# Kernel optimization log

Hardware: AMD Instinct MI355X
Metric: run time of the kernel (lower is better)

Reference implementation:

```python
import jax, jax.numpy as jnp
import numpy as np

B, L, H, E, R = 2, 512, 768, 512, 32768
H2 = H // 2


def setup_inputs() -> dict:
    key = jax.random.key(0)
    ks = jax.random.split(key, 16)
    s = 0.02
    inp = {
        "hidden_states": jax.random.normal(ks[0], (B, L, H), dtype=jnp.float32),
        "ent_start": jax.random.randint(ks[1], (B, E), 0, L, dtype=jnp.int32),
        "ent_label": jax.random.randint(ks[2], (B, E), 0, 3, dtype=jnp.int32),
        "rel_head": jax.random.randint(ks[3], (B, R), 0, E, dtype=jnp.int32),
        "rel_tail": jax.random.randint(ks[4], (B, R), 0, E, dtype=jnp.int32),
        "rel_label": jax.random.randint(ks[5], (B, R), 0, 2, dtype=jnp.int32),
        "entity_emb": jax.random.normal(ks[6], (3, H), dtype=jnp.float32) * s,
        "head_W1": jax.random.normal(ks[7], (2 * H, H), dtype=jnp.float32) * s,
        "head_b1": jnp.zeros((H,), dtype=jnp.float32),
        "head_W2": jax.random.normal(ks[8], (H, H2), dtype=jnp.float32) * s,
        "head_b2": jnp.zeros((H2,), dtype=jnp.float32),
        "tail_W1": jax.random.normal(ks[9], (2 * H, H), dtype=jnp.float32) * s,
        "tail_b1": jnp.zeros((H,), dtype=jnp.float32),
        "tail_W2": jax.random.normal(ks[10], (H, H2), dtype=jnp.float32) * s,
        "tail_b2": jnp.zeros((H2,), dtype=jnp.float32),
        "bil_W": jax.random.normal(ks[11], (2, H2, H2), dtype=jnp.float32) * s,
        "lin_W": jax.random.normal(ks[12], (2 * H2, 2), dtype=jnp.float32) * s,
        "lin_b": jnp.zeros((2,), dtype=jnp.float32),
    }
    return inp


def _mlp(x, W1, b1, W2, b2):
    # Linear -> ReLU -> (dropout=identity) -> Linear -> ReLU -> (dropout=identity)
    h = jax.nn.relu(jnp.einsum("brd,dh->brh", x, W1) + b1)
    return jax.nn.relu(jnp.einsum("brh,hk->brk", h, W2) + b2)


def reference(hidden_states, ent_start, ent_label, rel_head, rel_tail, rel_label,
              entity_emb, head_W1, head_b1, head_W2, head_b2,
              tail_W1, tail_b1, tail_W2, tail_b2, bil_W, lin_W, lin_b):
    # Gather entity start token index and label for each relation endpoint
    h_idx = jnp.take_along_axis(ent_start, rel_head, axis=1)  # [B,R]
    t_idx = jnp.take_along_axis(ent_start, rel_tail, axis=1)
    h_lab = jnp.take_along_axis(ent_label, rel_head, axis=1)
    t_lab = jnp.take_along_axis(ent_label, rel_tail, axis=1)

    # Gather hidden states at entity start positions: [B,R,H]
    h_tok = jnp.take_along_axis(hidden_states, h_idx[..., None], axis=1)
    t_tok = jnp.take_along_axis(hidden_states, t_idx[..., None], axis=1)

    head_repr = jnp.concatenate([h_tok, entity_emb[h_lab]], axis=-1)  # [B,R,2H]
    tail_repr = jnp.concatenate([t_tok, entity_emb[t_lab]], axis=-1)

    heads = _mlp(head_repr, head_W1, head_b1, head_W2, head_b2)  # [B,R,H2]
    tails = _mlp(tail_repr, tail_W1, tail_b1, tail_W2, tail_b2)

    # BiaffineAttention: bilinear(x1,x2) + linear(cat(x1,x2))
    bil = jnp.einsum("brd,ode,bre->bro", heads, bil_W, tails)  # [B,R,2]
    lin = jnp.einsum("brc,co->bro", jnp.concatenate([heads, tails], axis=-1), lin_W) + lin_b
    logits = bil + lin  # [B,R,2]

    # Per-doc mean cross-entropy, summed over docs (matches loss accumulation)
    logp = jax.nn.log_softmax(logits, axis=-1)
    ce = -jnp.take_along_axis(logp, rel_label[..., None], axis=-1)[..., 0]  # [B,R]
    loss = ce.mean(axis=-1).sum()

    return loss, logits.reshape(B * R, 2)
```

## Files before the change

### kernel.cpp

```cpp
#include <hip/hip_runtime.h>
#include <math.h>

#define BB 2
#define LL 512
#define HH 768
#define EE 512
#define RR 32768
#define H2 384
#define MM 1024

typedef __attribute__((ext_vector_type(8))) short     bf16x8;
typedef __attribute__((ext_vector_type(4))) float     f32x4;
typedef __attribute__((ext_vector_type(8))) unsigned short u16x8;

__device__ __forceinline__ unsigned short f2bf(float f) {
    unsigned int u = __float_as_uint(f);
    u = (u + 0x7FFFu + ((u >> 16) & 1u)) >> 16;
    return (unsigned short)u;
}

__global__ __launch_bounds__(256) void prep(
    const float* __restrict__ hW1, const float* __restrict__ tW1,
    const float* __restrict__ hW2, const float* __restrict__ tW2,
    const float* __restrict__ bilW,
    unsigned short* __restrict__ W1ht, unsigned short* __restrict__ W1tt,
    unsigned short* __restrict__ W2ht, unsigned short* __restrict__ W2tt,
    unsigned short* __restrict__ bW0t, unsigned short* __restrict__ bW1t,
    const float* __restrict__ hidden, const int* __restrict__ ent_start,
    const int* __restrict__ ent_label, const float* __restrict__ emb,
    const float* __restrict__ hb1, const float* __restrict__ tb1,
    unsigned short* __restrict__ Hbf, float* __restrict__ embc,
    float* __restrict__ hlin, float* __restrict__ tlin, float* __restrict__ out)
{
    __shared__ unsigned short T[32 * 40];
    __shared__ float red[4][192];
    const int bid = blockIdx.x;
    const int t = threadIdx.x;

    if (bid == 3064) {
        const float4 z = {0.f, 0.f, 0.f, 0.f};
        ((float4*)hlin)[t] = z; ((float4*)hlin)[256 + t] = z;
        ((float4*)tlin)[t] = z; ((float4*)tlin)[256 + t] = z;
        if (t == 0) out[0] = 0.f;
        return;
    }

    if (bid >= 3040) {
        const int eb = bid - 3040;
        const int tc = t & 63;
        const int kg = t >> 6;
        const int n = eb * 64 + tc;
        const float* W = (n < 768) ? hW1 : tW1;
        const int cc = (n < 768) ? n : n - 768;
        float a0 = 0.f, a1 = 0.f, a2 = 0.f;
        const int kbeg = kg * 192;
        #pragma unroll 8
        for (int k = kbeg; k < kbeg + 192; ++k) {
            const float w = W[(size_t)(768 + k) * 768 + cc];
            a0 += emb[k] * w;
            a1 += emb[768 + k] * w;
            a2 += emb[1536 + k] * w;
        }
        red[kg][0 * 64 + tc] = a0;
        red[kg][1 * 64 + tc] = a1;
        red[kg][2 * 64 + tc] = a2;
        __syncthreads();
        if (kg == 0) {
            const float b = (n < 768) ? hb1[n] : tb1[n - 768];
            #pragma unroll
            for (int l = 0; l < 3; ++l) {
                embc[l * 1536 + n] = b + red[0][l * 64 + tc] + red[1][l * 64 + tc]
                                       + red[2][l * 64 + tc] + red[3][l * 64 + tc];
            }
        }
        return;
    }

    if (bid >= 2016) {
        const int m = bid - 2016;
        if (t >= 96) return;
        const int b = m >> 9;
        const int idx = ent_start[m];
        const float4* s = (const float4*)(hidden + (size_t)(b * LL + idx) * HH);
        const float4 v0 = s[2 * t];
        const float4 v1 = s[2 * t + 1];
        u16x8 o;
        o[0] = f2bf(v0.x); o[1] = f2bf(v0.y); o[2] = f2bf(v0.z); o[3] = f2bf(v0.w);
        o[4] = f2bf(v1.x); o[5] = f2bf(v1.y); o[6] = f2bf(v1.z); o[7] = f2bf(v1.w);
        *(u16x8*)(Hbf + (size_t)m * 768 + 8 * t) = o;
        return;
    }

    const float* src; unsigned short* dst; int K, N, tile;
    if (bid < 576)       { src = hW1;            dst = W1ht; K = 768; N = 768; tile = bid; }
    else if (bid < 1152) { src = tW1;            dst = W1tt; K = 768; N = 768; tile = bid - 576; }
    else if (bid < 1440) { src = hW2;            dst = W2ht; K = 768; N = 384; tile = bid - 1152; }
    else if (bid < 1728) { src = tW2;            dst = W2tt; K = 768; N = 384; tile = bid - 1440; }
    else if (bid < 1872) { src = bilW;           dst = bW0t; K = 384; N = 384; tile = bid - 1728; }
    else                 { src = bilW + 384*384; dst = bW1t; K = 384; N = 384; tile = bid - 1872; }
    const int tn = N >> 5;
    const int n0 = (tile % tn) * 32;
    const int k0 = (tile / tn) * 32;

    const int r  = t >> 3;
    const int c4 = (t & 7) * 4;
    const float4 g = *(const float4*)(src + (size_t)(k0 + r) * N + n0 + c4);
    T[(c4 + 0) * 40 + r] = f2bf(g.x);
    T[(c4 + 1) * 40 + r] = f2bf(g.y);
    T[(c4 + 2) * 40 + r] = f2bf(g.z);
    T[(c4 + 3) * 40 + r] = f2bf(g.w);
    __syncthreads();
    const int n  = t >> 3;
    const int k4 = (t & 7) * 4;
    *(ushort4*)(dst + (size_t)(n0 + n) * K + k0 + k4) = *(ushort4*)&T[n * 40 + k4];
}

template<bool RELU, bool BIAS, bool EB, bool WF32, bool WBF16, bool O2, bool LIN>
__global__ __launch_bounds__(256) void gemm_mfma(
    const unsigned short* __restrict__ A, int lda, int aoff1,
    const unsigned short* __restrict__ Bt0, const unsigned short* __restrict__ Bt1,
    int ldb, int bt_mrow, int Nh,
    const float* __restrict__ bias0, const float* __restrict__ bias1,
    const float* __restrict__ embc, const int* __restrict__ labels,
    const float* __restrict__ linW, float* __restrict__ hlin, float* __restrict__ tlin,
    int K, float* __restrict__ Cf, unsigned short* __restrict__ Cb, int ldc)
{
    __shared__ unsigned short As[2][64 * 72];
    __shared__ unsigned short Bs[2][64 * 72];

    const int tid = threadIdx.x;
    const int n0 = blockIdx.x * 64;
    const int m0 = blockIdx.y * 64;
    const int hf = (n0 >= Nh) ? 1 : 0;
    const unsigned short* Bt = hf ? Bt1 : Bt0;
    const int nc0 = n0 - (hf ? Nh : 0);
    const int aoff = hf ? aoff1 : 0;

    const int sr = tid >> 2;
    const int sk = (tid & 3) * 16;

    const unsigned short* Ap = A + (size_t)(m0 + sr) * lda + aoff + sk;
    const unsigned short* Bp = Bt + (size_t)((m0 >> 9) * bt_mrow + nc0 + sr) * ldb + sk;

    const int lane = tid & 63;
    const int wave = tid >> 6;
    const int wm = (wave & 1) * 32;
    const int wn = (wave >> 1) * 32;
    const int l15 = lane & 15;
    const int quad = lane >> 4;

    f32x4 acc00 = {}, acc01 = {}, acc10 = {}, acc11 = {};

    u16x8 a0v = *(const u16x8*)(Ap);
    u16x8 a1v = *(const u16x8*)(Ap + 8);
    u16x8 b0v = *(const u16x8*)(Bp);
    u16x8 b1v = *(const u16x8*)(Bp + 8);
    const int swo = sr * 72 + sk;
    *(u16x8*)&As[0][swo] = a0v; *(u16x8*)&As[0][swo + 8] = a1v;
    *(u16x8*)&Bs[0][swo] = b0v; *(u16x8*)&Bs[0][swo + 8] = b1v;

    const int NT = K >> 6;
    const int aro = quad * 8;
    int cur = 0;
    for (int it = 0; it < NT; ++it) {
        if (it + 1 < NT) {
            const int ko = (it + 1) * 64;
            a0v = *(const u16x8*)(Ap + ko); a1v = *(const u16x8*)(Ap + ko + 8);
            b0v = *(const u16x8*)(Bp + ko); b1v = *(const u16x8*)(Bp + ko + 8);
        }
        asm volatile("s_waitcnt lgkmcnt(0)" ::: "memory");
        __builtin_amdgcn_s_barrier();
        __builtin_amdgcn_sched_barrier(0);
        const unsigned short* Ac = As[cur];
        const unsigned short* Bc = Bs[cur];
        const bf16x8 fa0 = *(const bf16x8*)&Ac[(wm + l15) * 72 + aro];
        const bf16x8 fa1 = *(const bf16x8*)&Ac[(wm + 16 + l15) * 72 + aro];
        const bf16x8 fb0 = *(const bf16x8*)&Bc[(wn + l15) * 72 + aro];
        const bf16x8 fb1 = *(const bf16x8*)&Bc[(wn + 16 + l15) * 72 + aro];
        const bf16x8 ga0 = *(const bf16x8*)&Ac[(wm + l15) * 72 + aro + 32];
        const bf16x8 ga1 = *(const bf16x8*)&Ac[(wm + 16 + l15) * 72 + aro + 32];
        const bf16x8 gb0 = *(const bf16x8*)&Bc[(wn + l15) * 72 + aro + 32];
        const bf16x8 gb1 = *(const bf16x8*)&Bc[(wn + 16 + l15) * 72 + aro + 32];
        acc00 = __builtin_amdgcn_mfma_f32_16x16x32_bf16(fa0, fb0, acc00, 0, 0, 0);
        acc01 = __builtin_amdgcn_mfma_f32_16x16x32_bf16(fa0, fb1, acc01, 0, 0, 0);
        acc10 = __builtin_amdgcn_mfma_f32_16x16x32_bf16(fa1, fb0, acc10, 0, 0, 0);
        acc11 = __builtin_amdgcn_mfma_f32_16x16x32_bf16(fa1, fb1, acc11, 0, 0, 0);
        acc00 = __builtin_amdgcn_mfma_f32_16x16x32_bf16(ga0, gb0, acc00, 0, 0, 0);
        acc01 = __builtin_amdgcn_mfma_f32_16x16x32_bf16(ga0, gb1, acc01, 0, 0, 0);
        acc10 = __builtin_amdgcn_mfma_f32_16x16x32_bf16(ga1, gb0, acc10, 0, 0, 0);
        acc11 = __builtin_amdgcn_mfma_f32_16x16x32_bf16(ga1, gb1, acc11, 0, 0, 0);
        if (it + 1 < NT) {
            unsigned short* Aw = &As[cur ^ 1][0];
            unsigned short* Bw = &Bs[cur ^ 1][0];
            *(u16x8*)&Aw[swo] = a0v; *(u16x8*)&Aw[swo + 8] = a1v;
            *(u16x8*)&Bw[swo] = b0v; *(u16x8*)&Bw[swo + 8] = b1v;
        }
        cur ^= 1;
    }

    float bias_v0 = 0.f, bias_v1 = 0.f;
    if (BIAS) {
        const float* bb = hf ? bias1 : bias0;
        bias_v0 = bb[nc0 + wn + l15];
        bias_v1 = bb[nc0 + wn + 16 + l15];
    }
    const int col0 = n0 + wn + l15;
    const int col1 = col0 + 16;
    int colw0 = col0, colw1 = col1;
    if (O2) {
        colw0 = 2 * (nc0 + wn + l15) + hf;
        colw1 = 2 * (nc0 + wn + 16 + l15) + hf;
    }
    float2 lw0 = {0.f, 0.f}, lw1 = {0.f, 0.f};
    float* lout = nullptr;
    if (LIN) {
        lw0 = ((const float2*)linW)[col0];
        lw1 = ((const float2*)linW)[col1];
        lout = hf ? tlin : hlin;
    }
    const f32x4 accs[2][2] = {{acc00, acc01}, {acc10, acc11}};
    #pragma unroll
    for (int mi = 0; mi < 2; ++mi) {
        #pragma unroll
        for (int r = 0; r < 4; ++r) {
            const int row = m0 + wm + mi * 16 + quad * 4 + r;
            float v0 = accs[mi][0][r];
            float v1 = accs[mi][1][r];
            if (BIAS) { v0 += bias_v0; v1 += bias_v1; }
            if (EB) {
                const int lab = labels[row];
                v0 += embc[lab * 1536 + col0];
                v1 += embc[lab * 1536 + col1];
            }
            if (RELU) { v0 = fmaxf(v0, 0.f); v1 = fmaxf(v1, 0.f); }
            if (WF32) {
                Cf[(size_t)row * ldc + colw0] = v0;
                Cf[(size_t)row * ldc + colw1] = v1;
            }
            if (WBF16) {
                Cb[(size_t)row * ldc + colw0] = f2bf(v0);
                Cb[(size_t)row * ldc + colw1] = f2bf(v1);
            }
            if (LIN) {
                float s0 = v0 * lw0.x + v1 * lw1.x;
                float s1 = v0 * lw0.y + v1 * lw1.y;
                #pragma unroll
                for (int o = 8; o >= 1; o >>= 1) {
                    s0 += __shfl_xor(s0, o, 64);
                    s1 += __shfl_xor(s1, o, 64);
                }
                if (l15 == 0) {
                    atomicAdd(&lout[2 * row],     s0);
                    atomicAdd(&lout[2 * row + 1], s1);
                }
            }
        }
    }
}

__global__ __launch_bounds__(256) void rel_gather(
    const float* __restrict__ Stab,
    const float* __restrict__ hlin, const float* __restrict__ tlin,
    const float* __restrict__ lin_b,
    const int* __restrict__ rel_head, const int* __restrict__ rel_tail,
    const int* __restrict__ rel_label,
    float* __restrict__ out)
{
    const int tid = threadIdx.x;
    const int i = blockIdx.x * 256 + tid;
    const int b = i >> 15;
    const int h = rel_head[i];
    const int t = rel_tail[i];
    const int lab = rel_label[i];
    const int mh = (b << 9) + h;
    const int mt = (b << 9) + t;

    const float2 hl = ((const float2*)hlin)[mh];
    const float2 tl = ((const float2*)tlin)[mt];
    const float2 zz = *(const float2*)(Stab + (size_t)mh * 1024 + 2 * t);
    const float z0 = zz.x + hl.x + tl.x + lin_b[0];
    const float z1 = zz.y + hl.y + tl.y + lin_b[1];
    out[1 + 2 * (size_t)i]     = z0;
    out[2 + 2 * (size_t)i]     = z1;

    const float mx = fmaxf(z0, z1);
    const float mn = fminf(z0, z1);
    const float lse = mx + log1pf(expf(mn - mx));
    float ce = lse - (lab ? z1 : z0);

    #pragma unroll
    for (int o = 32; o >= 1; o >>= 1) ce += __shfl_xor(ce, o, 64);
    __shared__ float wsum[4];
    if ((tid & 63) == 0) wsum[tid >> 6] = ce;
    __syncthreads();
    if (tid == 0) {
        const float bs = wsum[0] + wsum[1] + wsum[2] + wsum[3];
        atomicAdd(out, bs * (1.0f / (float)RR));
    }
}

extern "C" void kernel_launch(void* const* d_in, const int* in_sizes, int n_in,
                              void* d_out, int out_size, void* d_ws, size_t ws_size,
                              hipStream_t stream) {
    const float* hidden    = (const float*)d_in[0];
    const int*   ent_start = (const int*)d_in[1];
    const int*   ent_label = (const int*)d_in[2];
    const int*   rel_head  = (const int*)d_in[3];
    const int*   rel_tail  = (const int*)d_in[4];
    const int*   rel_label = (const int*)d_in[5];
    const float* emb       = (const float*)d_in[6];
    const float* head_W1   = (const float*)d_in[7];
    const float* head_b1   = (const float*)d_in[8];
    const float* head_W2   = (const float*)d_in[9];
    const float* head_b2   = (const float*)d_in[10];
    const float* tail_W1   = (const float*)d_in[11];
    const float* tail_b1   = (const float*)d_in[12];
    const float* tail_W2   = (const float*)d_in[13];
    const float* tail_b2   = (const float*)d_in[14];
    const float* bil_W     = (const float*)d_in[15];
    const float* lin_W     = (const float*)d_in[16];
    const float* lin_b     = (const float*)d_in[17];
    float* out = (float*)d_out;

    char* w = (char*)d_ws;
    auto carve = [&](size_t bytes) {
        char* p = w; w += (bytes + 255) & ~(size_t)255; return p;
    };
    unsigned short* Hbf  = (unsigned short*)carve((size_t)MM * 768 * 2);
    unsigned short* Y1bf = (unsigned short*)carve((size_t)MM * 1536 * 2);
    unsigned short* HTbf = (unsigned short*)carve((size_t)MM * 768 * 2);
    unsigned short* hWbf = (unsigned short*)carve((size_t)MM * 768 * 2);
    float*          Stab = (float*)carve((size_t)MM * 1024 * 4);
    unsigned short* W1ht = (unsigned short*)carve((size_t)768 * 768 * 2);
    unsigned short* W1tt = (unsigned short*)carve((size_t)768 * 768 * 2);
    unsigned short* W2ht = (unsigned short*)carve((size_t)384 * 768 * 2);
    unsigned short* W2tt = (unsigned short*)carve((size_t)384 * 768 * 2);
    unsigned short* bW0t = (unsigned short*)carve((size_t)384 * 384 * 2);
    unsigned short* bW1t = (unsigned short*)carve((size_t)384 * 384 * 2);
    float*          embc = (float*)carve((size_t)3 * 1536 * 4);
    float*          hlin = (float*)carve(2048 * 4);
    float*          tlin = (float*)carve(2048 * 4);

    prep<<<3065, 256, 0, stream>>>(
        head_W1, tail_W1, head_W2, tail_W2, bil_W,
        W1ht, W1tt, W2ht, W2tt, bW0t, bW1t,
        hidden, ent_start, ent_label, emb, head_b1, tail_b1, Hbf, embc,
        hlin, tlin, out);

    gemm_mfma<true, false, true, false, true, false, false>
        <<<dim3(24, 16), 256, 0, stream>>>(
        Hbf, 768, 0, W1ht, W1tt, 768, 0, 768, nullptr, nullptr, embc, ent_label,
        nullptr, nullptr, nullptr, 768, nullptr, Y1bf, 1536);

    gemm_mfma<true, true, false, false, true, false, true>
        <<<dim3(12, 16), 256, 0, stream>>>(
        Y1bf, 1536, 768, W2ht, W2tt, 768, 0, 384, head_b2, tail_b2, nullptr, nullptr,
        lin_W, hlin, tlin, 768, nullptr, HTbf, 768);

    gemm_mfma<false, false, false, false, true, false, false>
        <<<dim3(12, 16), 256, 0, stream>>>(
        HTbf, 768, 0, bW0t, bW1t, 384, 0, 384, nullptr, nullptr, nullptr, nullptr,
        nullptr, nullptr, nullptr, 384, nullptr, hWbf, 768);

    gemm_mfma<false, false, false, true, false, true, false>
        <<<dim3(16, 16), 256, 0, stream>>>(
        hWbf, 768, 384, HTbf + 384, HTbf + 384, 768, 512, 512,
        nullptr, nullptr, nullptr, nullptr,
        nullptr, nullptr, nullptr, 384, Stab, nullptr, 1024);

    rel_gather<<<256, 256, 0, stream>>>(Stab, hlin, tlin, lin_b,
                                        rel_head, rel_tail, rel_label, out);
}
```

Measured before the change: 142.5 us.

## Fuse all stages into one persistent kernel with grid-wide atomic barriers

```diff
diff --git a/kernel.cpp b/kernel.cpp
--- a/kernel.cpp
+++ b/kernel.cpp
@@ -8,6 +8,7 @@
 #define RR 32768
 #define H2 384
 #define MM 1024
+#define GRID 512
 
 typedef __attribute__((ext_vector_type(8))) short     bf16x8;
 typedef __attribute__((ext_vector_type(4))) float     f32x4;
@@ -19,25 +20,38 @@
     return (unsigned short)u;
 }
 
-__global__ __launch_bounds__(256) void prep(
-    const float* __restrict__ hW1, const float* __restrict__ tW1,
-    const float* __restrict__ hW2, const float* __restrict__ tW2,
-    const float* __restrict__ bilW,
-    unsigned short* __restrict__ W1ht, unsigned short* __restrict__ W1tt,
-    unsigned short* __restrict__ W2ht, unsigned short* __restrict__ W2tt,
-    unsigned short* __restrict__ bW0t, unsigned short* __restrict__ bW1t,
-    const float* __restrict__ hidden, const int* __restrict__ ent_start,
-    const int* __restrict__ ent_label, const float* __restrict__ emb,
-    const float* __restrict__ hb1, const float* __restrict__ tb1,
-    unsigned short* __restrict__ Hbf, float* __restrict__ embc,
-    float* __restrict__ hlin, float* __restrict__ tlin, float* __restrict__ out)
+__device__ __forceinline__ void gbar(unsigned* bars, int idx) {
+    __syncthreads();
+    if (threadIdx.x == 0) {
+        __threadfence();
+        if (atomicAdd(&bars[idx], 1u) + 1u < (unsigned)GRID) {
+            while (atomicAdd(&bars[idx], 0u) < (unsigned)GRID)
+                __builtin_amdgcn_s_sleep(4);
+        }
+        __threadfence();
+    }
+    __syncthreads();
+}
+
+__global__ __launch_bounds__(64) void init_bars(unsigned* bars) {
+    if (threadIdx.x < 8) bars[threadIdx.x] = 0u;
+}
+
+__device__ void prep_task(int task,
+    const float* hW1, const float* tW1, const float* hW2, const float* tW2,
+    const float* bilW,
+    unsigned short* W1ht, unsigned short* W1tt,
+    unsigned short* W2ht, unsigned short* W2tt,
+    unsigned short* bW0t, unsigned short* bW1t,
+    const float* hidden, const int* ent_start, const int* ent_label,
+    const float* emb, const float* hb1, const float* tb1,
+    unsigned short* Hbf, float* embc,
+    float* hlin, float* tlin, float* out,
+    unsigned short* SBu, float* SBf)
 {
-    __shared__ unsigned short T[32 * 40];
-    __shared__ float red[4][192];
-    const int bid = blockIdx.x;
     const int t = threadIdx.x;
 
-    if (bid == 3064) {
+    if (task == 3064) {
         const float4 z = {0.f, 0.f, 0.f, 0.f};
         ((float4*)hlin)[t] = z; ((float4*)hlin)[256 + t] = z;
         ((float4*)tlin)[t] = z; ((float4*)tlin)[256 + t] = z;
@@ -45,8 +59,8 @@
         return;
     }
 
-    if (bid >= 3040) {
-        const int eb = bid - 3040;
+    if (task >= 3040) {
+        const int eb = task - 3040;
         const int tc = t & 63;
         const int kg = t >> 6;
         const int n = eb * 64 + tc;
@@ -61,23 +75,24 @@
             a1 += emb[768 + k] * w;
             a2 += emb[1536 + k] * w;
         }
-        red[kg][0 * 64 + tc] = a0;
-        red[kg][1 * 64 + tc] = a1;
-        red[kg][2 * 64 + tc] = a2;
+        SBf[kg * 192 + 0 * 64 + tc] = a0;
+        SBf[kg * 192 + 1 * 64 + tc] = a1;
+        SBf[kg * 192 + 2 * 64 + tc] = a2;
         __syncthreads();
         if (kg == 0) {
             const float b = (n < 768) ? hb1[n] : tb1[n - 768];
             #pragma unroll
             for (int l = 0; l < 3; ++l) {
-                embc[l * 1536 + n] = b + red[0][l * 64 + tc] + red[1][l * 64 + tc]
-                                       + red[2][l * 64 + tc] + red[3][l * 64 + tc];
+                embc[l * 1536 + n] = b + SBf[0 * 192 + l * 64 + tc]
+                    + SBf[1 * 192 + l * 64 + tc] + SBf[2 * 192 + l * 64 + tc]
+                    + SBf[3 * 192 + l * 64 + tc];
             }
         }
         return;
     }
 
-    if (bid >= 2016) {
-        const int m = bid - 2016;
+    if (task >= 2016) {
+        const int m = task - 2016;
         if (t >= 96) return;
         const int b = m >> 9;
         const int idx = ent_start[m];
@@ -92,12 +107,12 @@
     }
 
     const float* src; unsigned short* dst; int K, N, tile;
-    if (bid < 576)       { src = hW1;            dst = W1ht; K = 768; N = 768; tile = bid; }
-    else if (bid < 1152) { src = tW1;            dst = W1tt; K = 768; N = 768; tile = bid - 576; }
-    else if (bid < 1440) { src = hW2;            dst = W2ht; K = 768; N = 384; tile = bid - 1152; }
-    else if (bid < 1728) { src = tW2;            dst = W2tt; K = 768; N = 384; tile = bid - 1440; }
-    else if (bid < 1872) { src = bilW;           dst = bW0t; K = 384; N = 384; tile = bid - 1728; }
-    else                 { src = bilW + 384*384; dst = bW1t; K = 384; N = 384; tile = bid - 1872; }
+    if (task < 576)       { src = hW1;            dst = W1ht; K = 768; N = 768; tile = task; }
+    else if (task < 1152) { src = tW1;            dst = W1tt; K = 768; N = 768; tile = task - 576; }
+    else if (task < 1440) { src = hW2;            dst = W2ht; K = 768; N = 384; tile = task - 1152; }
+    else if (task < 1728) { src = tW2;            dst = W2tt; K = 768; N = 384; tile = task - 1440; }
+    else if (task < 1872) { src = bilW;           dst = bW0t; K = 384; N = 384; tile = task - 1728; }
+    else                  { src = bilW + 384*384; dst = bW1t; K = 384; N = 384; tile = task - 1872; }
     const int tn = N >> 5;
     const int n0 = (tile % tn) * 32;
     const int k0 = (tile / tn) * 32;
@@ -105,32 +120,33 @@
     const int r  = t >> 3;
     const int c4 = (t & 7) * 4;
     const float4 g = *(const float4*)(src + (size_t)(k0 + r) * N + n0 + c4);
-    T[(c4 + 0) * 40 + r] = f2bf(g.x);
-    T[(c4 + 1) * 40 + r] = f2bf(g.y);
-    T[(c4 + 2) * 40 + r] = f2bf(g.z);
-    T[(c4 + 3) * 40 + r] = f2bf(g.w);
+    SBu[(c4 + 0) * 40 + r] = f2bf(g.x);
+    SBu[(c4 + 1) * 40 + r] = f2bf(g.y);
+    SBu[(c4 + 2) * 40 + r] = f2bf(g.z);
+    SBu[(c4 + 3) * 40 + r] = f2bf(g.w);
     __syncthreads();
     const int n  = t >> 3;
     const int k4 = (t & 7) * 4;
-    *(ushort4*)(dst + (size_t)(n0 + n) * K + k0 + k4) = *(ushort4*)&T[n * 40 + k4];
+    *(ushort4*)(dst + (size_t)(n0 + n) * K + k0 + k4) = *(ushort4*)&SBu[n * 40 + k4];
 }
 
 template<bool RELU, bool BIAS, bool EB, bool WF32, bool WBF16, bool O2, bool LIN>
-__global__ __launch_bounds__(256) void gemm_mfma(
+__device__ __forceinline__ void gemm_stage(
+    int ntiles, int nx,
     const unsigned short* __restrict__ A, int lda, int aoff1,
     const unsigned short* __restrict__ Bt0, const unsigned short* __restrict__ Bt1,
     int ldb, int bt_mrow, int Nh,
     const float* __restrict__ bias0, const float* __restrict__ bias1,
     const float* __restrict__ embc, const int* __restrict__ labels,
     const float* __restrict__ linW, float* __restrict__ hlin, float* __restrict__ tlin,
-    int K, float* __restrict__ Cf, unsigned short* __restrict__ Cb, int ldc)
+    int K, float* __restrict__ Cf, unsigned short* __restrict__ Cb, int ldc,
+    unsigned short* As, unsigned short* Bs)
 {
-    __shared__ unsigned short As[2][64 * 72];
-    __shared__ unsigned short Bs[2][64 * 72];
-
+    const int tile = blockIdx.x;
+    if (tile >= ntiles) return;
     const int tid = threadIdx.x;
-    const int n0 = blockIdx.x * 64;
-    const int m0 = blockIdx.y * 64;
+    const int n0 = (tile % nx) * 64;
+    const int m0 = (tile / nx) * 64;
     const int hf = (n0 >= Nh) ? 1 : 0;
     const unsigned short* Bt = hf ? Bt1 : Bt0;
     const int nc0 = n0 - (hf ? Nh : 0);
@@ -156,8 +172,8 @@
     u16x8 b0v = *(const u16x8*)(Bp);
     u16x8 b1v = *(const u16x8*)(Bp + 8);
     const int swo = sr * 72 + sk;
-    *(u16x8*)&As[0][swo] = a0v; *(u16x8*)&As[0][swo + 8] = a1v;
-    *(u16x8*)&Bs[0][swo] = b0v; *(u16x8*)&Bs[0][swo + 8] = b1v;
+    *(u16x8*)&As[swo] = a0v; *(u16x8*)&As[swo + 8] = a1v;
+    *(u16x8*)&Bs[swo] = b0v; *(u16x8*)&Bs[swo + 8] = b1v;
 
     const int NT = K >> 6;
     const int aro = quad * 8;
@@ -171,8 +187,8 @@
         asm volatile("s_waitcnt lgkmcnt(0)" ::: "memory");
         __builtin_amdgcn_s_barrier();
         __builtin_amdgcn_sched_barrier(0);
-        const unsigned short* Ac = As[cur];
-        const unsigned short* Bc = Bs[cur];
+        const unsigned short* Ac = As + cur * 4608;
+        const unsigned short* Bc = Bs + cur * 4608;
         const bf16x8 fa0 = *(const bf16x8*)&Ac[(wm + l15) * 72 + aro];
         const bf16x8 fa1 = *(const bf16x8*)&Ac[(wm + 16 + l15) * 72 + aro];
         const bf16x8 fb0 = *(const bf16x8*)&Bc[(wn + l15) * 72 + aro];
@@ -190,8 +206,8 @@
         acc10 = __builtin_amdgcn_mfma_f32_16x16x32_bf16(ga1, gb0, acc10, 0, 0, 0);
         acc11 = __builtin_amdgcn_mfma_f32_16x16x32_bf16(ga1, gb1, acc11, 0, 0, 0);
         if (it + 1 < NT) {
-            unsigned short* Aw = &As[cur ^ 1][0];
-            unsigned short* Bw = &Bs[cur ^ 1][0];
+            unsigned short* Aw = As + (cur ^ 1) * 4608;
+            unsigned short* Bw = Bs + (cur ^ 1) * 4608;
             *(u16x8*)&Aw[swo] = a0v; *(u16x8*)&Aw[swo + 8] = a1v;
             *(u16x8*)&Bw[swo] = b0v; *(u16x8*)&Bw[swo + 8] = b1v;
         }
@@ -258,44 +274,96 @@
     }
 }
 
-__global__ __launch_bounds__(256) void rel_gather(
-    const float* __restrict__ Stab,
-    const float* __restrict__ hlin, const float* __restrict__ tlin,
+__global__ __launch_bounds__(256) void fused(
+    const float* __restrict__ hidden, const int* __restrict__ ent_start,
+    const int* __restrict__ ent_label, const int* __restrict__ rel_head,
+    const int* __restrict__ rel_tail, const int* __restrict__ rel_label,
+    const float* __restrict__ emb,
+    const float* __restrict__ hW1, const float* __restrict__ hb1,
+    const float* __restrict__ hW2, const float* __restrict__ hb2,
+    const float* __restrict__ tW1, const float* __restrict__ tb1,
+    const float* __restrict__ tW2, const float* __restrict__ tb2,
+    const float* __restrict__ bilW, const float* __restrict__ linW,
     const float* __restrict__ lin_b,
-    const int* __restrict__ rel_head, const int* __restrict__ rel_tail,
-    const int* __restrict__ rel_label,
-    float* __restrict__ out)
+    unsigned short* __restrict__ Hbf, unsigned short* __restrict__ Y1bf,
+    unsigned short* __restrict__ HTbf, unsigned short* __restrict__ hWbf,
+    float* __restrict__ Stab,
+    unsigned short* __restrict__ W1ht, unsigned short* __restrict__ W1tt,
+    unsigned short* __restrict__ W2ht, unsigned short* __restrict__ W2tt,
+    unsigned short* __restrict__ bW0t, unsigned short* __restrict__ bW1t,
+    float* __restrict__ embc, float* __restrict__ hlin, float* __restrict__ tlin,
+    unsigned* __restrict__ bars, float* __restrict__ out)
 {
+    __shared__ __align__(16) unsigned short SB[2][2][4608];
+    unsigned short* As = &SB[0][0][0];
+    unsigned short* Bs = &SB[1][0][0];
     const int tid = threadIdx.x;
-    const int i = blockIdx.x * 256 + tid;
-    const int b = i >> 15;
-    const int h = rel_head[i];
-    const int t = rel_tail[i];
-    const int lab = rel_label[i];
-    const int mh = (b << 9) + h;
-    const int mt = (b << 9) + t;
-
-    const float2 hl = ((const float2*)hlin)[mh];
-    const float2 tl = ((const float2*)tlin)[mt];
-    const float2 zz = *(const float2*)(Stab + (size_t)mh * 1024 + 2 * t);
-    const float z0 = zz.x + hl.x + tl.x + lin_b[0];
-    const float z1 = zz.y + hl.y + tl.y + lin_b[1];
-    out[1 + 2 * (size_t)i]     = z0;
-    out[2 + 2 * (size_t)i]     = z1;
-
-    const float mx = fmaxf(z0, z1);
-    const float mn = fminf(z0, z1);
-    const float lse = mx + log1pf(expf(mn - mx));
-    float ce = lse - (lab ? z1 : z0);
-
-    #pragma unroll
-    for (int o = 32; o >= 1; o >>= 1) ce += __shfl_xor(ce, o, 64);
-    __shared__ float wsum[4];
-    if ((tid & 63) == 0) wsum[tid >> 6] = ce;
-    __syncthreads();
-    if (tid == 0) {
-        const float bs = wsum[0] + wsum[1] + wsum[2] + wsum[3];
-        atomicAdd(out, bs * (1.0f / (float)RR));
+
+    for (int task = blockIdx.x; task < 3065; task += GRID) {
+        prep_task(task, hW1, tW1, hW2, tW2, bilW,
+                  W1ht, W1tt, W2ht, W2tt, bW0t, bW1t,
+                  hidden, ent_start, ent_label, emb, hb1, tb1,
+                  Hbf, embc, hlin, tlin, out,
+                  As, (float*)As);
+        __syncthreads();
+    }
+    gbar(bars, 0);
+
+    gemm_stage<true, false, true, false, true, false, false>(
+        384, 24, Hbf, 768, 0, W1ht, W1tt, 768, 0, 768,
+        nullptr, nullptr, embc, ent_label, nullptr, nullptr, nullptr,
+        768, nullptr, Y1bf, 1536, As, Bs);
+    gbar(bars, 1);
+
+    gemm_stage<true, true, false, false, true, false, true>(
+        192, 12, Y1bf, 1536, 768, W2ht, W2tt, 768, 0, 384,
+        hb2, tb2, nullptr, nullptr, linW, hlin, tlin,
+        768, nullptr, HTbf, 768, As, Bs);
+    gbar(bars, 2);
+
+    gemm_stage<false, false, false, false, true, false, false>(
+        192, 12, HTbf, 768, 0, bW0t, bW1t, 384, 0, 384,
+        nullptr, nullptr, nullptr, nullptr, nullptr, nullptr, nullptr,
+        384, nullptr, hWbf, 768, As, Bs);
+    gbar(bars, 3);
+
+    gemm_stage<false, false, false, true, false, true, false>(
+        256, 16, hWbf, 768, 384, HTbf + 384, HTbf + 384, 768, 512, 512,
+        nullptr, nullptr, nullptr, nullptr, nullptr, nullptr, nullptr,
+        384, Stab, nullptr, 1024, As, Bs);
+    gbar(bars, 4);
+
+    {
+        float ce = 0.f;
+        if (tid < 128) {
+            const int i = blockIdx.x * 128 + tid;
+            const int b = i >> 15;
+            const int h = rel_head[i];
+            const int t = rel_tail[i];
+            const int lab = rel_label[i];
+            const int mh = (b << 9) + h;
+            const int mt = (b << 9) + t;
+            const float2 hl = ((const float2*)hlin)[mh];
+            const float2 tl = ((const float2*)tlin)[mt];
+            const float2 zz = *(const float2*)(Stab + (size_t)mh * 1024 + 2 * t);
+            const float z0 = zz.x + hl.x + tl.x + lin_b[0];
+            const float z1 = zz.y + hl.y + tl.y + lin_b[1];
+            out[1 + 2 * (size_t)i] = z0;
+            out[2 + 2 * (size_t)i] = z1;
+            const float mx = fmaxf(z0, z1);
+            const float mn = fminf(z0, z1);
+            const float lse = mx + log1pf(expf(mn - mx));
+            ce = lse - (lab ? z1 : z0);
+        }
+        #pragma unroll
+        for (int o = 32; o >= 1; o >>= 1) ce += __shfl_xor(ce, o, 64);
+        float* wsum = (float*)As;
+        if ((tid & 63) == 0) wsum[tid >> 6] = ce;
+        __syncthreads();
+        if (tid == 0) {
+            const float bs = wsum[0] + wsum[1] + wsum[2] + wsum[3];
+            atomicAdd(out, bs * (1.0f / (float)RR));
+        }
     }
 }
 
@@ -340,34 +408,16 @@
     float*          embc = (float*)carve((size_t)3 * 1536 * 4);
     float*          hlin = (float*)carve(2048 * 4);
     float*          tlin = (float*)carve(2048 * 4);
-
-    prep<<<3065, 256, 0, stream>>>(
-        head_W1, tail_W1, head_W2, tail_W2, bil_W,
+    unsigned*       bars = (unsigned*)carve(8 * 4);
+
+    init_bars<<<1, 64, 0, stream>>>(bars);
+
+    fused<<<GRID, 256, 0, stream>>>(
+        hidden, ent_start, ent_label, rel_head, rel_tail, rel_label, emb,
+        head_W1, head_b1, head_W2, head_b2,
+        tail_W1, tail_b1, tail_W2, tail_b2,
+        bil_W, lin_W, lin_b,
+        Hbf, Y1bf, HTbf, hWbf, Stab,
         W1ht, W1tt, W2ht, W2tt, bW0t, bW1t,
-        hidden, ent_start, ent_label, emb, head_b1, tail_b1, Hbf, embc,
-        hlin, tlin, out);
-
-    gemm_mfma<true, false, true, false, true, false, false>
-        <<<dim3(24, 16), 256, 0, stream>>>(
-        Hbf, 768, 0, W1ht, W1tt, 768, 0, 768, nullptr, nullptr, embc, ent_label,
-        nullptr, nullptr, nullptr, 768, nullptr, Y1bf, 1536);
-
-    gemm_mfma<true, true, false, false, true, false, true>
-        <<<dim3(12, 16), 256, 0, stream>>>(
-        Y1bf, 1536, 768, W2ht, W2tt, 768, 0, 384, head_b2, tail_b2, nullptr, nullptr,
-        lin_W, hlin, tlin, 768, nullptr, HTbf, 768);
-
-    gemm_mfma<false, false, false, false, true, false, false>
-        <<<dim3(12, 16), 256, 0, stream>>>(
-        HTbf, 768, 0, bW0t, bW1t, 384, 0, 384, nullptr, nullptr, nullptr, nullptr,
-        nullptr, nullptr, nullptr, 384, nullptr, hWbf, 768);
-
-    gemm_mfma<false, false, false, true, false, true, false>
-        <<<dim3(16, 16), 256, 0, stream>>>(
-        hWbf, 768, 384, HTbf + 384, HTbf + 384, 768, 512, 512,
-        nullptr, nullptr, nullptr, nullptr,
-        nullptr, nullptr, nullptr, 384, Stab, nullptr, 1024);
-
-    rel_gather<<<256, 256, 0, stream>>>(Stab, hlin, tlin, lin_b,
-                                        rel_head, rel_tail, rel_label, out);
-}
+        embc, hlin, tlin, bars, out);
+}
```

After: 385.2 us. +170.4%, slower.

## Replace all-pairs bilinear score GEMM with per-relation dot products

Applied to the files above, without the earlier changes.

```diff
diff --git a/kernel.cpp b/kernel.cpp
--- a/kernel.cpp
+++ b/kernel.cpp
@@ -17,6 +17,9 @@
     unsigned int u = __float_as_uint(f);
     u = (u + 0x7FFFu + ((u >> 16) & 1u)) >> 16;
     return (unsigned short)u;
+}
+__device__ __forceinline__ float bf2f(unsigned short u) {
+    return __uint_as_float((unsigned)u << 16);
 }
 
 __global__ __launch_bounds__(256) void prep(
@@ -115,18 +118,18 @@
     *(ushort4*)(dst + (size_t)(n0 + n) * K + k0 + k4) = *(ushort4*)&T[n * 40 + k4];
 }
 
-template<bool RELU, bool BIAS, bool EB, bool WF32, bool WBF16, bool O2, bool LIN>
+template<bool RELU, bool BIAS, bool EB, bool LIN>
 __global__ __launch_bounds__(256) void gemm_mfma(
     const unsigned short* __restrict__ A, int lda, int aoff1,
     const unsigned short* __restrict__ Bt0, const unsigned short* __restrict__ Bt1,
-    int ldb, int bt_mrow, int Nh,
+    int ldb, int Nh,
     const float* __restrict__ bias0, const float* __restrict__ bias1,
     const float* __restrict__ embc, const int* __restrict__ labels,
     const float* __restrict__ linW, float* __restrict__ hlin, float* __restrict__ tlin,
-    int K, float* __restrict__ Cf, unsigned short* __restrict__ Cb, int ldc)
+    int K, unsigned short* __restrict__ Cb, int ldc)
 {
-    __shared__ unsigned short As[2][64 * 72];
-    __shared__ unsigned short Bs[2][64 * 72];
+    __shared__ __align__(16) unsigned short As[2][64 * 72];
+    __shared__ __align__(16) unsigned short Bs[2][64 * 72];
 
     const int tid = threadIdx.x;
     const int n0 = blockIdx.x * 64;
@@ -140,7 +143,7 @@
     const int sk = (tid & 3) * 16;
 
     const unsigned short* Ap = A + (size_t)(m0 + sr) * lda + aoff + sk;
-    const unsigned short* Bp = Bt + (size_t)((m0 >> 9) * bt_mrow + nc0 + sr) * ldb + sk;
+    const unsigned short* Bp = Bt + (size_t)(nc0 + sr) * ldb + sk;
 
     const int lane = tid & 63;
     const int wave = tid >> 6;
@@ -190,8 +193,8 @@
         acc10 = __builtin_amdgcn_mfma_f32_16x16x32_bf16(ga1, gb0, acc10, 0, 0, 0);
         acc11 = __builtin_amdgcn_mfma_f32_16x16x32_bf16(ga1, gb1, acc11, 0, 0, 0);
         if (it + 1 < NT) {
-            unsigned short* Aw = &As[cur ^ 1][0];
-            unsigned short* Bw = &Bs[cur ^ 1][0];
+            unsigned short* Aw = As[cur ^ 1];
+            unsigned short* Bw = Bs[cur ^ 1];
             *(u16x8*)&Aw[swo] = a0v; *(u16x8*)&Aw[swo + 8] = a1v;
             *(u16x8*)&Bw[swo] = b0v; *(u16x8*)&Bw[swo + 8] = b1v;
         }
@@ -206,11 +209,6 @@
     }
     const int col0 = n0 + wn + l15;
     const int col1 = col0 + 16;
-    int colw0 = col0, colw1 = col1;
-    if (O2) {
-        colw0 = 2 * (nc0 + wn + l15) + hf;
-        colw1 = 2 * (nc0 + wn + 16 + l15) + hf;
-    }
     float2 lw0 = {0.f, 0.f}, lw1 = {0.f, 0.f};
     float* lout = nullptr;
     if (LIN) {
@@ -233,14 +231,8 @@
                 v1 += embc[lab * 1536 + col1];
             }
             if (RELU) { v0 = fmaxf(v0, 0.f); v1 = fmaxf(v1, 0.f); }
-            if (WF32) {
-                Cf[(size_t)row * ldc + colw0] = v0;
-                Cf[(size_t)row * ldc + colw1] = v1;
-            }
-            if (WBF16) {
-                Cb[(size_t)row * ldc + colw0] = f2bf(v0);
-                Cb[(size_t)row * ldc + colw1] = f2bf(v1);
-            }
+            Cb[(size_t)row * ldc + col0] = f2bf(v0);
+            Cb[(size_t)row * ldc + col1] = f2bf(v1);
             if (LIN) {
                 float s0 = v0 * lw0.x + v1 * lw1.x;
                 float s1 = v0 * lw0.y + v1 * lw1.y;
@@ -258,8 +250,8 @@
     }
 }
 
-__global__ __launch_bounds__(256) void rel_gather(
-    const float* __restrict__ Stab,
+__global__ __launch_bounds__(256) void rel_score(
+    const unsigned short* __restrict__ hWbf, const unsigned short* __restrict__ HTbf,
     const float* __restrict__ hlin, const float* __restrict__ tlin,
     const float* __restrict__ lin_b,
     const int* __restrict__ rel_head, const int* __restrict__ rel_tail,
@@ -267,36 +259,51 @@
     float* __restrict__ out)
 {
     const int tid = threadIdx.x;
-    const int i = blockIdx.x * 256 + tid;
-    const int b = i >> 15;
-    const int h = rel_head[i];
-    const int t = rel_tail[i];
-    const int lab = rel_label[i];
-    const int mh = (b << 9) + h;
-    const int mt = (b << 9) + t;
-
-    const float2 hl = ((const float2*)hlin)[mh];
-    const float2 tl = ((const float2*)tlin)[mt];
-    const float2 zz = *(const float2*)(Stab + (size_t)mh * 1024 + 2 * t);
-    const float z0 = zz.x + hl.x + tl.x + lin_b[0];
-    const float z1 = zz.y + hl.y + tl.y + lin_b[1];
-    out[1 + 2 * (size_t)i]     = z0;
-    out[2 + 2 * (size_t)i]     = z1;
-
-    const float mx = fmaxf(z0, z1);
-    const float mn = fminf(z0, z1);
-    const float lse = mx + log1pf(expf(mn - mx));
-    float ce = lse - (lab ? z1 : z0);
-
-    #pragma unroll
-    for (int o = 32; o >= 1; o >>= 1) ce += __shfl_xor(ce, o, 64);
+    const int lane = tid & 63;
+    const int wave = tid >> 6;
+    const float lb0 = lin_b[0], lb1 = lin_b[1];
+    const int base = (blockIdx.x * 4 + wave) * 8;
+    float ce_acc = 0.f;
+    for (int r = 0; r < 8; ++r) {
+        const int i = base + r;
+        const int b = i >> 15;
+        const int h = rel_head[i];
+        const int t = rel_tail[i];
+        const int mh = (b << 9) + h;
+        const int mt = (b << 9) + t;
+        const unsigned short* hw = hWbf + (size_t)mh * 768;
+        const unsigned short* tp = HTbf + (size_t)mt * 768 + 384;
+        float a0 = 0.f, a1 = 0.f;
+        #pragma unroll
+        for (int j = 0; j < 6; ++j) {
+            const int d = j * 64 + lane;
+            const float tv = bf2f(tp[d]);
+            a0 += bf2f(hw[d])       * tv;
+            a1 += bf2f(hw[384 + d]) * tv;
+        }
+        #pragma unroll
+        for (int o = 32; o >= 1; o >>= 1) {
+            a0 += __shfl_xor(a0, o, 64);
+            a1 += __shfl_xor(a1, o, 64);
+        }
+        if (lane == 0) {
+            const float2 hl = ((const float2*)hlin)[mh];
+            const float2 tl = ((const float2*)tlin)[mt];
+            const float z0 = a0 + hl.x + tl.x + lb0;
+            const float z1 = a1 + hl.y + tl.y + lb1;
+            out[1 + 2 * (size_t)i] = z0;
+            out[2 + 2 * (size_t)i] = z1;
+            const float mx = fmaxf(z0, z1);
+            const float mn = fminf(z0, z1);
+            const int lab = rel_label[i];
+            ce_acc += mx + log1pf(expf(mn - mx)) - (lab ? z1 : z0);
+        }
+    }
     __shared__ float wsum[4];
-    if ((tid & 63) == 0) wsum[tid >> 6] = ce;
+    if (lane == 0) wsum[wave] = ce_acc;
     __syncthreads();
-    if (tid == 0) {
-        const float bs = wsum[0] + wsum[1] + wsum[2] + wsum[3];
-        atomicAdd(out, bs * (1.0f / (float)RR));
-    }
+    if (tid == 0)
+        atomicAdd(out, (wsum[0] + wsum[1] + wsum[2] + wsum[3]) * (1.0f / (float)RR));
 }
 
 extern "C" void kernel_launch(void* const* d_in, const int* in_sizes, int n_in,
@@ -330,7 +337,6 @@
     unsigned short* Y1bf = (unsigned short*)carve((size_t)MM * 1536 * 2);
     unsigned short* HTbf = (unsigned short*)carve((size_t)MM * 768 * 2);
     unsigned short* hWbf = (unsigned short*)carve((size_t)MM * 768 * 2);
-    float*          Stab = (float*)carve((size_t)MM * 1024 * 4);
     unsigned short* W1ht = (unsigned short*)carve((size_t)768 * 768 * 2);
     unsigned short* W1tt = (unsigned short*)carve((size_t)768 * 768 * 2);
     unsigned short* W2ht = (unsigned short*)carve((size_t)384 * 768 * 2);
@@ -347,27 +353,18 @@
         hidden, ent_start, ent_label, emb, head_b1, tail_b1, Hbf, embc,
         hlin, tlin, out);
 
-    gemm_mfma<true, false, true, false, true, false, false>
-        <<<dim3(24, 16), 256, 0, stream>>>(
-        Hbf, 768, 0, W1ht, W1tt, 768, 0, 768, nullptr, nullptr, embc, ent_label,
-        nullptr, nullptr, nullptr, 768, nullptr, Y1bf, 1536);
-
-    gemm_mfma<true, true, false, false, true, false, true>
-        <<<dim3(12, 16), 256, 0, stream>>>(
-        Y1bf, 1536, 768, W2ht, W2tt, 768, 0, 384, head_b2, tail_b2, nullptr, nullptr,
-        lin_W, hlin, tlin, 768, nullptr, HTbf, 768);
-
-    gemm_mfma<false, false, false, false, true, false, false>
-        <<<dim3(12, 16), 256, 0, stream>>>(
-        HTbf, 768, 0, bW0t, bW1t, 384, 0, 384, nullptr, nullptr, nullptr, nullptr,
-        nullptr, nullptr, nullptr, 384, nullptr, hWbf, 768);
-
-    gemm_mfma<false, false, false, true, false, true, false>
-        <<<dim3(16, 16), 256, 0, stream>>>(
-        hWbf, 768, 384, HTbf + 384, HTbf + 384, 768, 512, 512,
-        nullptr, nullptr, nullptr, nullptr,
-        nullptr, nullptr, nullptr, 384, Stab, nullptr, 1024);
-
-    rel_gather<<<256, 256, 0, stream>>>(Stab, hlin, tlin, lin_b,
+    gemm_mfma<true, false, true, false><<<dim3(24, 16), 256, 0, stream>>>(
+        Hbf, 768, 0, W1ht, W1tt, 768, 768, nullptr, nullptr, embc, ent_label,
+        nullptr, nullptr, nullptr, 768, Y1bf, 1536);
+
+    gemm_mfma<true, true, false, true><<<dim3(12, 16), 256, 0, stream>>>(
+        Y1bf, 1536, 768, W2ht, W2tt, 768, 384, head_b2, tail_b2, nullptr, nullptr,
+        lin_W, hlin, tlin, 768, HTbf, 768);
+
+    gemm_mfma<false, false, false, false><<<dim3(12, 16), 256, 0, stream>>>(
+        HTbf, 768, 0, bW0t, bW1t, 384, 384, nullptr, nullptr, nullptr, nullptr,
+        nullptr, nullptr, nullptr, 384, hWbf, 768);
+
+    rel_score<<<2048, 256, 0, stream>>>(hWbf, HTbf, hlin, tlin, lin_b,
                                         rel_head, rel_tail, rel_label, out);
 }
```

Result: slower. 169.5 us (+19.0%).
